# Optimization experiments

Measured on AMD Instinct MI355X. Metric: run time of the kernel, lower is better.

The kernel has to match this reference:

```python
import jax, jax.numpy as jnp
import numpy as np

EPS = 1e-12


def setup_inputs() -> dict:
    key = jax.random.key(0)
    k1, k2, k3 = jax.random.split(key, 3)
    n, d, n_ids = 4096, 2048, 64
    modal1_inputs = jax.random.normal(k1, (n, d), dtype=jnp.float32)
    modal2_inputs = jax.random.normal(k2, (n, d), dtype=jnp.float32)
    targets = jax.random.randint(k3, (n,), 0, n_ids, dtype=jnp.int64)
    return {
        "modal1_inputs": modal1_inputs,
        "modal2_inputs": modal2_inputs,
        "targets": targets,
        "margin": 0.3,
    }


def reference(modal1_inputs, modal2_inputs, targets, margin):
    # Pairwise euclidean distance between modal1 rows and modal2 rows: [n, n]
    sq1 = jnp.sum(modal1_inputs * modal1_inputs, axis=1, keepdims=True)  # [n,1]
    sq2 = jnp.sum(modal2_inputs * modal2_inputs, axis=1, keepdims=True)  # [n,1]
    dist = sq1 + sq2.T - 2.0 * (modal1_inputs @ modal2_inputs.T)
    dist = jnp.sqrt(jnp.clip(dist, EPS, None))

    # Same-identity mask: [n, n]
    mask = targets[:, None] == targets[None, :]

    # Hard positive (max over same-id) / hard negative (min over diff-id) per row
    neg_inf = jnp.asarray(-jnp.inf, dist.dtype)
    pos_inf = jnp.asarray(jnp.inf, dist.dtype)
    dist_ap = jnp.max(jnp.where(mask, dist, neg_inf), axis=1)  # [n]
    dist_an = jnp.min(jnp.where(mask, pos_inf, dist), axis=1)  # [n]

    # MarginRankingLoss(dist_an, dist_ap, y=1) with mean reduction:
    # mean(max(0, -(dist_an - dist_ap) + margin))
    loss = jnp.mean(jnp.maximum(dist_ap - dist_an + margin, 0.0))
    prec = jnp.mean((dist_an > dist_ap).astype(jnp.float32))
    return loss, prec
```

## Files before the change

kernel.cpp:

```cpp
#include <hip/hip_runtime.h>
#include <hip/hip_bf16.h>
#include <stdint.h>

#define N_ROWS 4096
#define DIM    2048
#define BK     64
#define EPSF   1e-12f

typedef __bf16 bf16x8 __attribute__((ext_vector_type(8)));
typedef float  f32x4  __attribute__((ext_vector_type(4)));

typedef __attribute__((address_space(1))) void gv_t;
typedef __attribute__((address_space(3))) void lv_t;

__device__ __forceinline__ void gload_lds16(const void* g, void* l) {
    __builtin_amdgcn_global_load_lds((gv_t*)g, (lv_t*)l, 16, 0, 0);
}

__device__ __forceinline__ unsigned short f2bf(float f) {
    unsigned u = __float_as_uint(f);
    return (unsigned short)((u + 0x7FFFu + ((u >> 16) & 1u)) >> 16);
}

__global__ __launch_bounds__(256) void prep_kernel(
    const float* __restrict__ m1, const float* __restrict__ m2,
    unsigned short* __restrict__ abf, unsigned short* __restrict__ bbf,
    float* __restrict__ sq1, float* __restrict__ sq2,
    unsigned* __restrict__ ap_bits, unsigned* __restrict__ an_bits) {
    const int blk = blockIdx.x;
    const bool isB = blk >= N_ROWS;
    const int r = isB ? blk - N_ROWS : blk;
    const float* src = (isB ? m2 : m1) + (size_t)r * DIM;
    unsigned short* dst = (isB ? bbf : abf) + (size_t)r * DIM;
    const int tid = threadIdx.x;

    const float4* s4 = (const float4*)src;
    float4 v0 = s4[tid];
    float4 v1 = s4[tid + 256];
    float acc = v0.x*v0.x + v0.y*v0.y + v0.z*v0.z + v0.w*v0.w
              + v1.x*v1.x + v1.y*v1.y + v1.z*v1.z + v1.w*v1.w;

    uint2 p0, p1;
    p0.x = (unsigned)f2bf(v0.x) | ((unsigned)f2bf(v0.y) << 16);
    p0.y = (unsigned)f2bf(v0.z) | ((unsigned)f2bf(v0.w) << 16);
    p1.x = (unsigned)f2bf(v1.x) | ((unsigned)f2bf(v1.y) << 16);
    p1.y = (unsigned)f2bf(v1.z) | ((unsigned)f2bf(v1.w) << 16);
    *(uint2*)(dst + tid * 4)         = p0;
    *(uint2*)(dst + (tid + 256) * 4) = p1;

    for (int s = 32; s > 0; s >>= 1) acc += __shfl_down(acc, s);
    __shared__ float red[4];
    if ((tid & 63) == 0) red[tid >> 6] = acc;
    __syncthreads();
    if (tid == 0) {
        float* sq = isB ? sq2 : sq1;
        sq[r] = red[0] + red[1] + red[2] + red[3];
        if (!isB) {
            ap_bits[r] = 0u;
            an_bits[r] = 0x7f800000u;
        }
    }
}

__global__ __launch_bounds__(256) void dist_gemm_kernel(
    const unsigned short* __restrict__ A, const unsigned short* __restrict__ B,
    const float* __restrict__ sq1, const float* __restrict__ sq2,
    const int* __restrict__ tgt,
    unsigned* __restrict__ ap_bits, unsigned* __restrict__ an_bits) {
    __shared__ unsigned short As[128 * BK];
    __shared__ unsigned short Bs[128 * BK];

    const int tid  = threadIdx.x;
    const int w    = tid >> 6;
    const int lane = tid & 63;
    const int wr   = w >> 1, wc = w & 1;
    const int l15  = lane & 15, lhi = lane >> 4;
    const int brow = blockIdx.y * 128, bcol = blockIdx.x * 128;

    const int srow  = lane >> 3;
    const int skoff = (lane & 7) * 8;

    f32x4 acc[4][4] = {};

    for (int kt = 0; kt < DIM; kt += BK) {
#pragma unroll
        for (int c = 0; c < 4; ++c) {
            const int chunk = w + c * 4;
            const unsigned short* ga = A + (size_t)(brow + chunk * 8 + srow) * DIM + kt + skoff;
            gload_lds16(ga, &As[chunk * 512]);
            const unsigned short* gb = B + (size_t)(bcol + chunk * 8 + srow) * DIM + kt + skoff;
            gload_lds16(gb, &Bs[chunk * 512]);
        }

        __syncthreads();

#pragma unroll
        for (int kk = 0; kk < 2; ++kk) {
            bf16x8 af[4], bfr[4];
#pragma unroll
            for (int m = 0; m < 4; ++m)
                af[m] = *(const bf16x8*)&As[(wr * 64 + m * 16 + l15) * BK + kk * 32 + lhi * 8];
#pragma unroll
            for (int n = 0; n < 4; ++n)
                bfr[n] = *(const bf16x8*)&Bs[(wc * 64 + n * 16 + l15) * BK + kk * 32 + lhi * 8];

#pragma unroll
            for (int m = 0; m < 4; ++m)
#pragma unroll
                for (int n = 0; n < 4; ++n)
                    acc[m][n] = __builtin_amdgcn_mfma_f32_16x16x32_bf16(af[m], bfr[n], acc[m][n], 0, 0, 0);
        }

        __syncthreads();
    }

    int   tcol[4];
    float s2c[4];
#pragma unroll
    for (int n = 0; n < 4; ++n) {
        int col = bcol + wc * 64 + n * 16 + l15;
        tcol[n] = tgt[col];
        s2c[n]  = sq2[col];
    }
    const float INF = __uint_as_float(0x7f800000u);
#pragma unroll
    for (int m = 0; m < 4; ++m) {
#pragma unroll
        for (int reg = 0; reg < 4; ++reg) {
            int   row  = brow + wr * 64 + m * 16 + lhi * 4 + reg;
            int   trow = tgt[row];
            float s1   = sq1[row];
            float pmax = 0.0f;
            float nmin = INF;
#pragma unroll
            for (int n = 0; n < 4; ++n) {
                float d2 = s1 + s2c[n] - 2.0f * acc[m][n][reg];
                float dd = sqrtf(fmaxf(d2, EPSF));
                if (trow == tcol[n]) pmax = fmaxf(pmax, dd);
                else                 nmin = fminf(nmin, dd);
            }
#pragma unroll
            for (int s = 1; s < 16; s <<= 1) {
                pmax = fmaxf(pmax, __shfl_xor(pmax, s));
                nmin = fminf(nmin, __shfl_xor(nmin, s));
            }
            if (l15 == 0) {
                atomicMax(&ap_bits[row], __float_as_uint(pmax));
                atomicMin(&an_bits[row], __float_as_uint(nmin));
            }
        }
    }
}

__global__ __launch_bounds__(256) void finalize_kernel(
    const unsigned* __restrict__ ap_bits, const unsigned* __restrict__ an_bits,
    const float* __restrict__ marginp, float* __restrict__ out) {
    const int tid = threadIdx.x;
    const float margin = marginp[0];
    float ls = 0.f, ps = 0.f;
    for (int i = tid; i < N_ROWS; i += 256) {
        float a = __uint_as_float(ap_bits[i]);
        float b = __uint_as_float(an_bits[i]);
        ls += fmaxf(a - b + margin, 0.0f);
        ps += (b > a) ? 1.0f : 0.0f;
    }
    for (int s = 32; s > 0; s >>= 1) {
        ls += __shfl_down(ls, s);
        ps += __shfl_down(ps, s);
    }
    __shared__ float sl[4], sp[4];
    if ((tid & 63) == 0) { sl[tid >> 6] = ls; sp[tid >> 6] = ps; }
    __syncthreads();
    if (tid == 0) {
        ls = sl[0] + sl[1] + sl[2] + sl[3];
        ps = sp[0] + sp[1] + sp[2] + sp[3];
        out[0] = ls / (float)N_ROWS;
        out[1] = ps / (float)N_ROWS;
    }
}

extern "C" void kernel_launch(void* const* d_in, const int* in_sizes, int n_in,
                              void* d_out, int out_size, void* d_ws, size_t ws_size,
                              hipStream_t stream) {
    const float* m1  = (const float*)d_in[0];
    const float* m2  = (const float*)d_in[1];
    const int*   tgt = (const int*)d_in[2];
    const float* mrg = (const float*)d_in[3];

    char* ws = (char*)d_ws;
    unsigned short* abf = (unsigned short*)ws;
    unsigned short* bbf = (unsigned short*)(ws + 16777216);
    float*    sq1 = (float*)(ws + 33554432);
    float*    sq2 = (float*)(ws + 33554432 + 16384);
    unsigned* ap  = (unsigned*)(ws + 33554432 + 32768);
    unsigned* an  = (unsigned*)(ws + 33554432 + 49152);

    float* outp = (float*)d_out;

    prep_kernel<<<2 * N_ROWS, 256, 0, stream>>>(m1, m2, abf, bbf, sq1, sq2, ap, an);
    dim3 grid(N_ROWS / 128, N_ROWS / 128);
    dist_gemm_kernel<<<grid, 256, 0, stream>>>(abf, bbf, sq1, sq2, tgt, ap, an);
    finalize_kernel<<<1, 256, 0, stream>>>(ap, an, mrg, outp);
}
```

Baseline: 222.2 us.

## Restructure distance GEMM into 256x256 double-buffered, LDS-swizzled, phase-interleaved pipeline

Rewrites the bf16 distance GEMM to use 256x256 block tiles with 8 waves and double-buffered LDS. Each K-step is split into four MFMA phases, and the next tile's global-to-LDS loads are issued between them under explicit vmcnt waits and raw barriers, with s_setprio raised around the MFMA bursts. It also adds an XOR swizzle on LDS columns to avoid bank conflicts and a block-index remap for L2 locality. The goal is to hide load latency and raise data reuse per block. In exchange it uses a large LDS footprint, fills only one block per CU, and relies on hand-tuned waitcnt counts that must stay consistent.

```diff
diff --git a/kernel.cpp b/kernel.cpp
--- a/kernel.cpp
+++ b/kernel.cpp
@@ -4,7 +4,7 @@
 
 #define N_ROWS 4096
 #define DIM    2048
-#define BK     64
+#define NT     (DIM / 64)
 #define EPSF   1e-12f
 
 typedef __bf16 bf16x8 __attribute__((ext_vector_type(8)));
@@ -62,56 +62,116 @@
     }
 }
 
-__global__ __launch_bounds__(256) void dist_gemm_kernel(
+__global__ __launch_bounds__(512) void dist_gemm_kernel(
     const unsigned short* __restrict__ A, const unsigned short* __restrict__ B,
     const float* __restrict__ sq1, const float* __restrict__ sq2,
     const int* __restrict__ tgt,
     unsigned* __restrict__ ap_bits, unsigned* __restrict__ an_bits) {
-    __shared__ unsigned short As[128 * BK];
-    __shared__ unsigned short Bs[128 * BK];
+    __shared__ unsigned short As[2][256 * 64];
+    __shared__ unsigned short Bs[2][256 * 64];
 
     const int tid  = threadIdx.x;
     const int w    = tid >> 6;
     const int lane = tid & 63;
-    const int wr   = w >> 1, wc = w & 1;
+    const int wr   = w >> 2, wc = w & 3;
     const int l15  = lane & 15, lhi = lane >> 4;
-    const int brow = blockIdx.y * 128, bcol = blockIdx.x * 128;
-
-    const int srow  = lane >> 3;
-    const int skoff = (lane & 7) * 8;
-
-    f32x4 acc[4][4] = {};
-
-    for (int kt = 0; kt < DIM; kt += BK) {
-#pragma unroll
-        for (int c = 0; c < 4; ++c) {
-            const int chunk = w + c * 4;
-            const unsigned short* ga = A + (size_t)(brow + chunk * 8 + srow) * DIM + kt + skoff;
-            gload_lds16(ga, &As[chunk * 512]);
-            const unsigned short* gb = B + (size_t)(bcol + chunk * 8 + srow) * DIM + kt + skoff;
-            gload_lds16(gb, &Bs[chunk * 512]);
+    const int swz8 = (l15 & 7) * 8;
+
+    const int bid  = blockIdx.y * 16 + blockIdx.x;
+    const int swz  = (bid & 7) * 32 + (bid >> 3);
+    const int brow = (swz >> 4) * 256, bcol = (swz & 15) * 256;
+
+    const int srow = w * 8 + (lane >> 3);
+    const int scol = ((lane & 7) ^ (lane >> 3)) * 8;
+
+#define STAGE_A(buf, c, kt1) gload_lds16(                                        \
+        A + (size_t)(brow + (c) * 64 + srow) * DIM + (kt1) + scol,               \
+        &As[buf][((c) * 64 + w * 8) * 64])
+#define STAGE_B(buf, c, kt1) gload_lds16(                                        \
+        B + (size_t)(bcol + (c) * 64 + srow) * DIM + (kt1) + scol,               \
+        &Bs[buf][((c) * 64 + w * 8) * 64])
+#define LDA(m, kk) (*(const bf16x8*)&As[cur][(wr * 128 + (m) * 16 + l15) * 64 + (((kk) * 32 + lhi * 8) ^ swz8)])
+#define LDB(n, kk) (*(const bf16x8*)&Bs[cur][(wc * 64 + (n) * 16 + l15) * 64 + (((kk) * 32 + lhi * 8) ^ swz8)])
+#define BAR() asm volatile("s_barrier" ::: "memory")
+#define MFMA(a, b, c) __builtin_amdgcn_mfma_f32_16x16x32_bf16((a), (b), (c), 0, 0, 0)
+
+    f32x4 acc[8][4] = {};
+
+    STAGE_B(0, 0, 0); STAGE_B(0, 1, 0); STAGE_B(0, 2, 0); STAGE_B(0, 3, 0);
+    STAGE_A(0, 0, 0); STAGE_A(0, 2, 0); STAGE_A(0, 1, 0); STAGE_A(0, 3, 0);
+    asm volatile("s_waitcnt vmcnt(2)" ::: "memory");
+    BAR();
+
+    for (int t = 0; t < NT; ++t) {
+        const int  cur  = t & 1, nxt = cur ^ 1;
+        const int  kt1  = (t + 1) * 64;
+        const bool more = (t + 1 < NT);
+        bf16x8 af[4][2], bn[4][2];
+
+#pragma unroll
+        for (int m = 0; m < 4; ++m) { af[m][0] = LDA(m, 0); af[m][1] = LDA(m, 1); }
+#pragma unroll
+        for (int n = 0; n < 2; ++n) { bn[n][0] = LDB(n, 0); bn[n][1] = LDB(n, 1); }
+        if (more) { STAGE_B(nxt, 0, kt1); STAGE_B(nxt, 1, kt1); }
+        BAR();
+        __builtin_amdgcn_s_setprio(1);
+#pragma unroll
+        for (int m = 0; m < 4; ++m)
+#pragma unroll
+            for (int n = 0; n < 2; ++n) {
+                acc[m][n] = MFMA(af[m][0], bn[n][0], acc[m][n]);
+                acc[m][n] = MFMA(af[m][1], bn[n][1], acc[m][n]);
+            }
+        __builtin_amdgcn_s_setprio(0);
+        BAR();
+
+#pragma unroll
+        for (int n = 0; n < 2; ++n) { bn[n + 2][0] = LDB(n + 2, 0); bn[n + 2][1] = LDB(n + 2, 1); }
+        if (more) { STAGE_B(nxt, 2, kt1); STAGE_B(nxt, 3, kt1); }
+        if (t == NT - 1) { asm volatile("s_waitcnt vmcnt(0)" ::: "memory"); }
+        else             { asm volatile("s_waitcnt vmcnt(4)" ::: "memory"); }
+        BAR();
+        __builtin_amdgcn_s_setprio(1);
+#pragma unroll
+        for (int m = 0; m < 4; ++m)
+#pragma unroll
+            for (int n = 0; n < 2; ++n) {
+                acc[m][n + 2] = MFMA(af[m][0], bn[n + 2][0], acc[m][n + 2]);
+                acc[m][n + 2] = MFMA(af[m][1], bn[n + 2][1], acc[m][n + 2]);
+            }
+        __builtin_amdgcn_s_setprio(0);
+        BAR();
+
+#pragma unroll
+        for (int m = 0; m < 4; ++m) { af[m][0] = LDA(m + 4, 0); af[m][1] = LDA(m + 4, 1); }
+        if (more) { STAGE_A(nxt, 0, kt1); STAGE_A(nxt, 2, kt1); }
+        BAR();
+        __builtin_amdgcn_s_setprio(1);
+#pragma unroll
+        for (int m = 0; m < 4; ++m)
+#pragma unroll
+            for (int n = 0; n < 2; ++n) {
+                acc[m + 4][n] = MFMA(af[m][0], bn[n][0], acc[m + 4][n]);
+                acc[m + 4][n] = MFMA(af[m][1], bn[n][1], acc[m + 4][n]);
+            }
+        __builtin_amdgcn_s_setprio(0);
+        BAR();
+
+        if (more) {
+            STAGE_A(nxt, 1, kt1); STAGE_A(nxt, 3, kt1);
+            asm volatile("s_waitcnt vmcnt(2)" ::: "memory");
         }
-
-        __syncthreads();
-
-#pragma unroll
-        for (int kk = 0; kk < 2; ++kk) {
-            bf16x8 af[4], bfr[4];
-#pragma unroll
-            for (int m = 0; m < 4; ++m)
-                af[m] = *(const bf16x8*)&As[(wr * 64 + m * 16 + l15) * BK + kk * 32 + lhi * 8];
-#pragma unroll
-            for (int n = 0; n < 4; ++n)
-                bfr[n] = *(const bf16x8*)&Bs[(wc * 64 + n * 16 + l15) * BK + kk * 32 + lhi * 8];
-
-#pragma unroll
-            for (int m = 0; m < 4; ++m)
-#pragma unroll
-                for (int n = 0; n < 4; ++n)
-                    acc[m][n] = __builtin_amdgcn_mfma_f32_16x16x32_bf16(af[m], bfr[n], acc[m][n], 0, 0, 0);
-        }
-
-        __syncthreads();
+        BAR();
+        __builtin_amdgcn_s_setprio(1);
+#pragma unroll
+        for (int m = 0; m < 4; ++m)
+#pragma unroll
+            for (int n = 0; n < 2; ++n) {
+                acc[m + 4][n + 2] = MFMA(af[m][0], bn[n + 2][0], acc[m + 4][n + 2]);
+                acc[m + 4][n + 2] = MFMA(af[m][1], bn[n + 2][1], acc[m + 4][n + 2]);
+            }
+        __builtin_amdgcn_s_setprio(0);
+        BAR();
     }
 
     int   tcol[4];
@@ -124,10 +184,10 @@
     }
     const float INF = __uint_as_float(0x7f800000u);
 #pragma unroll
-    for (int m = 0; m < 4; ++m) {
+    for (int m = 0; m < 8; ++m) {
 #pragma unroll
         for (int reg = 0; reg < 4; ++reg) {
-            int   row  = brow + wr * 64 + m * 16 + lhi * 4 + reg;
+            int   row  = brow + wr * 128 + m * 16 + lhi * 4 + reg;
             int   trow = tgt[row];
             float s1   = sq1[row];
             float pmax = 0.0f;
@@ -150,6 +210,12 @@
             }
         }
     }
+#undef STAGE_A
+#undef STAGE_B
+#undef LDA
+#undef LDB
+#undef BAR
+#undef MFMA
 }
 
 __global__ __launch_bounds__(256) void finalize_kernel(
@@ -198,7 +264,7 @@
     float* outp = (float*)d_out;
 
     prep_kernel<<<2 * N_ROWS, 256, 0, stream>>>(m1, m2, abf, bbf, sq1, sq2, ap, an);
-    dim3 grid(N_ROWS / 128, N_ROWS / 128);
-    dist_gemm_kernel<<<grid, 256, 0, stream>>>(abf, bbf, sq1, sq2, tgt, ap, an);
+    dim3 grid(N_ROWS / 256, N_ROWS / 256);
+    dist_gemm_kernel<<<grid, 512, 0, stream>>>(abf, bbf, sq1, sq2, tgt, ap, an);
     finalize_kernel<<<1, 256, 0, stream>>>(ap, an, mrg, outp);
 }
```

Result: faster. 183.6 us (-17.4%).
